# Kernel optimization log

Hardware: AMD Instinct MI355X
Metric: run time of the kernel (lower is better)

Reference implementation:

```python
import jax, jax.numpy as jnp
import numpy as np

MARGIN = 2.0
EPS = 1e-6  # F.pairwise_distance default: norm of (x1 - x2 + eps)

N, D = 4096, 768


def setup_inputs() -> dict:
    key = jax.random.key(0)
    k1, k2, k3 = jax.random.split(key, 3)
    image_embedding = jax.random.normal(k1, (N, D), dtype=jnp.float32)
    text_embedding = jax.random.normal(k2, (N, D), dtype=jnp.float32)
    ground_truth = jax.random.randint(k3, (N, N), 0, 2, dtype=jnp.int32)
    return {
        "image_embedding": image_embedding,
        "text_embedding": text_embedding,
        "ground_truth": ground_truth,
    }


def reference(image_embedding, text_embedding, ground_truth):
    d = image_embedding.shape[1]
    # Pairwise squared distance with pairwise_distance's +eps on the diff:
    # ||a - b + eps||^2 = ||a||^2 + ||b||^2 - 2 a.b + 2 eps (sum a - sum b) + d eps^2
    sa = jnp.sum(image_embedding * image_embedding, axis=1)   # [n]
    sb = jnp.sum(text_embedding * text_embedding, axis=1)     # [n]
    dot = image_embedding @ text_embedding.T                  # [n, n]
    ra = jnp.sum(image_embedding, axis=1)                     # [n]
    rb = jnp.sum(text_embedding, axis=1)                      # [n]
    sq = (sa[:, None] + sb[None, :] - 2.0 * dot
          + 2.0 * EPS * (ra[:, None] - rb[None, :]) + d * EPS * EPS)
    dist = jnp.sqrt(jnp.maximum(sq, 0.0))                     # [n, n]
    label = ground_truth.astype(dist.dtype)
    hinge = jnp.maximum(MARGIN - dist, 0.0)
    loss = jnp.mean((1.0 - label) * dist * dist + label * hinge * hinge)
    return loss
```

## Files before the change

### kernel.cpp

```cpp
#include <hip/hip_runtime.h>
#include <hip/hip_bf16.h>
#include <stdint.h>
#include <stddef.h>


#define NROWS 4096
#define DIM   768
#define BM    128
#define BN    128
#define BKE   128
#define MARGIN 2.0f
#define EPSV   1e-6f

typedef float f32x4 __attribute__((ext_vector_type(4)));
typedef long  lng2  __attribute__((ext_vector_type(2)));
typedef unsigned long long u64;
typedef unsigned char fp8_t;


__global__ __launch_bounds__(256) void prologue_kernel(
    const float* __restrict__ A, const float* __restrict__ B,
    const int* __restrict__ gt,
    fp8_t* __restrict__ Af8, fp8_t* __restrict__ Bf8,
    float* __restrict__ sa, float* __restrict__ sb,
    float* __restrict__ ra, float* __restrict__ rb,
    u64* __restrict__ gtp, float* __restrict__ out)
{
    const int tid  = threadIdx.x;
    const int wave = tid >> 6;
    const int lane = tid & 63;
    const int bx   = blockIdx.x;

    if (bx == 0 && tid == 0) out[0] = 0.0f;

    if (bx < 2048) {
        const int isB  = bx >= 1024;
        const int row  = (bx & 1023) * 4 + wave;
        const float* X = isB ? B : A;
        fp8_t* Xb      = isB ? Bf8 : Af8;
        float* sdst    = isB ? sb : sa;
        float* rdst    = isB ? rb : ra;

        const float4* xr = (const float4*)(X + (size_t)row * DIM);
        unsigned int* xb = (unsigned int*)(Xb + (size_t)row * DIM);

        float sum = 0.0f, sq = 0.0f;
        #pragma unroll
        for (int jb = 0; jb < 3; ++jb) {
            float4 v = xr[lane + 64 * jb];
            int pk = 0;
            pk = __builtin_amdgcn_cvt_pk_fp8_f32(v.x, v.y, pk, false);
            pk = __builtin_amdgcn_cvt_pk_fp8_f32(v.z, v.w, pk, true);
            const int e4  = lane + 64 * jb;
            const int seg = e4 >> 5;
            const int e   = (e4 & 31) * 4;
            const int kk  = e >> 5;
            const int q   = (e >> 3) & 3;
            const int jj  = e & 7;
            const int pos = ((kk >> 1) * 4 + q) * 16 + (kk & 1) * 8 + jj;
            xb[seg * 32 + (pos >> 2)] = (unsigned int)pk;
            sum += (v.x + v.y) + (v.z + v.w);
            sq  += v.x * v.x + v.y * v.y + v.z * v.z + v.w * v.w;
        }
        #pragma unroll
        for (int off = 32; off > 0; off >>= 1) {
            sum += __shfl_down(sum, off);
            sq  += __shfl_down(sq,  off);
        }
        if (lane == 0) { rdst[row] = sum; sdst[row] = sq; }
    } else {
        const int wid = (bx - 2048) * 4 + wave;
        const size_t base = (size_t)wid * 8;
        int v[8];
        #pragma unroll
        for (int i = 0; i < 8; ++i)
            v[i] = gt[base * 64 + (size_t)i * 64 + lane];
        u64 mine = 0;
        #pragma unroll
        for (int i = 0; i < 8; ++i) {
            const u64 m = __ballot(v[i] != 0);
            if (lane == i) mine = m;
        }
        if (lane < 8) gtp[base + lane] = mine;
    }
}

__global__ __launch_bounds__(256, 4) void loss_kernel(
    const fp8_t* __restrict__ A, const fp8_t* __restrict__ B,
    const float* __restrict__ sa, const float* __restrict__ sb,
    const float* __restrict__ ra, const float* __restrict__ rb,
    const uint2* __restrict__ gtp, float* __restrict__ out)
{
    __shared__ __align__(16) fp8_t As[BM * BKE];
    __shared__ __align__(16) fp8_t Bs[BN * BKE];

    const int tid  = threadIdx.x;
    const int wave = tid >> 6;
    const int lane = tid & 63;
    const int m0 = blockIdx.y * BM;
    const int n0 = blockIdx.x * BN;

    f32x4 acc[4][4] = {};

    const int fr = lane & 15;
    const int q  = lane >> 4;
    const int wm = (wave >> 1) * 64;
    const int wn = (wave & 1) * 64;

    const int srow = lane >> 3;
    const int sp   = lane & 7;

    for (int k0 = 0; k0 < DIM; k0 += BKE) {
        __syncthreads();
        #pragma unroll
        for (int j = 0; j < 4; ++j) {
            const int c0  = wave * 256 + j * 64;
            const int row = (c0 >> 3) + srow;
            const int gcx = sp ^ (row & 7);
            const fp8_t* ga = A + (size_t)(m0 + row) * DIM + k0 + gcx * 16;
            __builtin_amdgcn_global_load_lds(
                (const __attribute__((address_space(1))) void*)ga,
                (__attribute__((address_space(3))) void*)(As + c0 * 16),
                16, 0, 0);
        }
        #pragma unroll
        for (int j = 0; j < 4; ++j) {
            const int c0  = wave * 256 + j * 64;
            const int row = (c0 >> 3) + srow;
            const int gcx = sp ^ (row & 7);
            const fp8_t* gb = B + (size_t)(n0 + row) * DIM + k0 + gcx * 16;
            __builtin_amdgcn_global_load_lds(
                (const __attribute__((address_space(1))) void*)gb,
                (__attribute__((address_space(3))) void*)(Bs + c0 * 16),
                16, 0, 0);
        }
        __syncthreads();

        #pragma unroll
        for (int kk2 = 0; kk2 < 2; ++kk2) {
            const int c = kk2 * 4 + q;
            lng2 ap[4], bp[4];
            #pragma unroll
            for (int i = 0; i < 4; ++i) {
                const int ar = wm + i * 16 + fr;
                const int br = wn + i * 16 + fr;
                ap[i] = *(const lng2*)(As + ar * BKE + ((c ^ (ar & 7)) * 16));
                bp[i] = *(const lng2*)(Bs + br * BKE + ((c ^ (br & 7)) * 16));
            }
            #pragma unroll
            for (int mi = 0; mi < 4; ++mi)
                #pragma unroll
                for (int ni = 0; ni < 4; ++ni)
                    acc[mi][ni] = __builtin_amdgcn_mfma_f32_16x16x32_fp8_fp8(
                        ap[mi][0], bp[ni][0], acc[mi][ni], 0, 0, 0);
            #pragma unroll
            for (int mi = 0; mi < 4; ++mi)
                #pragma unroll
                for (int ni = 0; ni < 4; ++ni)
                    acc[mi][ni] = __builtin_amdgcn_mfma_f32_16x16x32_fp8_fp8(
                        ap[mi][1], bp[ni][1], acc[mi][ni], 0, 0, 0);
        }
    }

    const int cq = lane & 15;
    const int rq = (lane >> 4) * 4;
    const int cb = (n0 + wn) >> 6;

    float cc[4];
    #pragma unroll
    for (int ni = 0; ni < 4; ++ni) {
        const int col = n0 + wn + ni * 16 + cq;
        cc[ni] = sb[col] - 2.0f * EPSV * rb[col];
    }

    float local = 0.0f;
    #pragma unroll
    for (int mi = 0; mi < 4; ++mi) {
        #pragma unroll
        for (int rr = 0; rr < 4; ++rr) {
            const int row = m0 + wm + mi * 16 + rq + rr;
            const float crr = sa[row] + 2.0f * EPSV * ra[row]
                            + (float)DIM * EPSV * EPSV;
            const uint2 w = gtp[(size_t)row * (NROWS / 64) + cb];
            #pragma unroll
            for (int ni = 0; ni < 4; ++ni) {
                const float d2 = (crr + cc[ni]) - 2.0f * acc[mi][ni][rr];
                const unsigned wd = (ni < 2) ? w.x : w.y;
                const float gf = (float)((wd >> (cq + (ni & 1) * 16)) & 1u);
                float contrib = d2 - gf * d2;
                if (__builtin_expect(d2 < 4.0f, 0)) {
                    const float d2c  = fmaxf(d2, 0.0f);
                    const float dist = sqrtf(d2c);
                    const float h    = fmaxf(MARGIN - dist, 0.0f);
                    contrib = (1.0f - gf) * d2c + gf * h * h;
                }
                local += contrib;
            }
        }
    }

    #pragma unroll
    for (int off = 32; off > 0; off >>= 1) local += __shfl_down(local, off);

    float* redp = (float*)As;
    __syncthreads();
    if (lane == 0) redp[wave] = local;
    __syncthreads();
    if (tid == 0) {
        const float s = (redp[0] + redp[1]) + (redp[2] + redp[3]);
        atomicAdd(out, s * (1.0f / (4096.0f * 4096.0f)));
    }
}

extern "C" void kernel_launch(void* const* d_in, const int* in_sizes, int n_in,
                              void* d_out, int out_size, void* d_ws, size_t ws_size,
                              hipStream_t stream)
{
    const float* A  = (const float*)d_in[0];
    const float* B  = (const float*)d_in[1];
    const int*   gt = (const int*)d_in[2];
    float* out = (float*)d_out;

    char* ws = (char*)d_ws;
    const size_t NB8 = (size_t)NROWS * DIM;
    fp8_t* Af8 = (fp8_t*)(ws);
    fp8_t* Bf8 = (fp8_t*)(ws + NB8);
    float* sa = (float*)(ws + 2 * NB8);
    float* sb = (float*)(ws + 2 * NB8 + 16384);
    float* ra = (float*)(ws + 2 * NB8 + 32768);
    float* rb = (float*)(ws + 2 * NB8 + 49152);
    u64* gtp  = (u64*)(ws + 2 * NB8 + 65536);

    prologue_kernel<<<dim3(10240), 256, 0, stream>>>(
        A, B, gt, Af8, Bf8, sa, sb, ra, rb, gtp, out);
    loss_kernel<<<dim3(NROWS / BN, NROWS / BM), 256, 0, stream>>>(
        Af8, Bf8, sa, sb, ra, rb, (const uint2*)gtp, out);
}
```

Baseline: 136.9 us.

## Fuse ground-truth bitmask packing into the loss GEMM kernel's K loop

Moves the int32 ground-truth to bitmask packing out of the prologue kernel and into the loss kernel. Each block now loads its own 128x128 tile of labels during the first four K iterations, overlapping those loads with the fp8 tile loads, and stores per-row bitmasks in shared memory. The prologue shrinks to the embedding conversion only. This removes the separate packed-mask round trip through global memory, but adds register pressure and ballot work inside the GEMM loop.

```diff
diff --git a/kernel.cpp b/kernel.cpp
--- a/kernel.cpp
+++ b/kernel.cpp
@@ -20,11 +20,10 @@
 
 __global__ __launch_bounds__(256) void prologue_kernel(
     const float* __restrict__ A, const float* __restrict__ B,
-    const int* __restrict__ gt,
     fp8_t* __restrict__ Af8, fp8_t* __restrict__ Bf8,
     float* __restrict__ sa, float* __restrict__ sb,
     float* __restrict__ ra, float* __restrict__ rb,
-    u64* __restrict__ gtp, float* __restrict__ out)
+    float* __restrict__ out)
 {
     const int tid  = threadIdx.x;
     const int wave = tid >> 6;
@@ -33,66 +32,51 @@
 
     if (bx == 0 && tid == 0) out[0] = 0.0f;
 
-    if (bx < 2048) {
-        const int isB  = bx >= 1024;
-        const int row  = (bx & 1023) * 4 + wave;
-        const float* X = isB ? B : A;
-        fp8_t* Xb      = isB ? Bf8 : Af8;
-        float* sdst    = isB ? sb : sa;
-        float* rdst    = isB ? rb : ra;
-
-        const float4* xr = (const float4*)(X + (size_t)row * DIM);
-        unsigned int* xb = (unsigned int*)(Xb + (size_t)row * DIM);
-
-        float sum = 0.0f, sq = 0.0f;
-        #pragma unroll
-        for (int jb = 0; jb < 3; ++jb) {
-            float4 v = xr[lane + 64 * jb];
-            int pk = 0;
-            pk = __builtin_amdgcn_cvt_pk_fp8_f32(v.x, v.y, pk, false);
-            pk = __builtin_amdgcn_cvt_pk_fp8_f32(v.z, v.w, pk, true);
-            const int e4  = lane + 64 * jb;
-            const int seg = e4 >> 5;
-            const int e   = (e4 & 31) * 4;
-            const int kk  = e >> 5;
-            const int q   = (e >> 3) & 3;
-            const int jj  = e & 7;
-            const int pos = ((kk >> 1) * 4 + q) * 16 + (kk & 1) * 8 + jj;
-            xb[seg * 32 + (pos >> 2)] = (unsigned int)pk;
-            sum += (v.x + v.y) + (v.z + v.w);
-            sq  += v.x * v.x + v.y * v.y + v.z * v.z + v.w * v.w;
-        }
-        #pragma unroll
-        for (int off = 32; off > 0; off >>= 1) {
-            sum += __shfl_down(sum, off);
-            sq  += __shfl_down(sq,  off);
-        }
-        if (lane == 0) { rdst[row] = sum; sdst[row] = sq; }
-    } else {
-        const int wid = (bx - 2048) * 4 + wave;
-        const size_t base = (size_t)wid * 8;
-        int v[8];
-        #pragma unroll
-        for (int i = 0; i < 8; ++i)
-            v[i] = gt[base * 64 + (size_t)i * 64 + lane];
-        u64 mine = 0;
-        #pragma unroll
-        for (int i = 0; i < 8; ++i) {
-            const u64 m = __ballot(v[i] != 0);
-            if (lane == i) mine = m;
-        }
-        if (lane < 8) gtp[base + lane] = mine;
-    }
+    const int isB  = bx >= 1024;
+    const int row  = (bx & 1023) * 4 + wave;
+    const float* X = isB ? B : A;
+    fp8_t* Xb      = isB ? Bf8 : Af8;
+    float* sdst    = isB ? sb : sa;
+    float* rdst    = isB ? rb : ra;
+
+    const float4* xr = (const float4*)(X + (size_t)row * DIM);
+    unsigned int* xb = (unsigned int*)(Xb + (size_t)row * DIM);
+
+    float sum = 0.0f, sq = 0.0f;
+    #pragma unroll
+    for (int jb = 0; jb < 3; ++jb) {
+        float4 v = xr[lane + 64 * jb];
+        int pk = 0;
+        pk = __builtin_amdgcn_cvt_pk_fp8_f32(v.x, v.y, pk, false);
+        pk = __builtin_amdgcn_cvt_pk_fp8_f32(v.z, v.w, pk, true);
+        const int e4  = lane + 64 * jb;
+        const int seg = e4 >> 5;
+        const int e   = (e4 & 31) * 4;
+        const int kk  = e >> 5;
+        const int q   = (e >> 3) & 3;
+        const int jj  = e & 7;
+        const int pos = ((kk >> 1) * 4 + q) * 16 + (kk & 1) * 8 + jj;
+        xb[seg * 32 + (pos >> 2)] = (unsigned int)pk;
+        sum += (v.x + v.y) + (v.z + v.w);
+        sq  += v.x * v.x + v.y * v.y + v.z * v.z + v.w * v.w;
+    }
+    #pragma unroll
+    for (int off = 32; off > 0; off >>= 1) {
+        sum += __shfl_down(sum, off);
+        sq  += __shfl_down(sq,  off);
+    }
+    if (lane == 0) { rdst[row] = sum; sdst[row] = sq; }
 }
 
 __global__ __launch_bounds__(256, 4) void loss_kernel(
     const fp8_t* __restrict__ A, const fp8_t* __restrict__ B,
     const float* __restrict__ sa, const float* __restrict__ sb,
     const float* __restrict__ ra, const float* __restrict__ rb,
-    const uint2* __restrict__ gtp, float* __restrict__ out)
+    const int* __restrict__ gt, float* __restrict__ out)
 {
     __shared__ __align__(16) fp8_t As[BM * BKE];
     __shared__ __align__(16) fp8_t Bs[BN * BKE];
+    __shared__ unsigned int gmask[BM][4];
 
     const int tid  = threadIdx.x;
     const int wave = tid >> 6;
@@ -110,7 +94,20 @@
     const int srow = lane >> 3;
     const int sp   = lane & 7;
 
-    for (int k0 = 0; k0 < DIM; k0 += BKE) {
+    for (int kb = 0; kb < DIM / BKE; ++kb) {
+        const int k0 = kb * BKE;
+        const int rbase = kb * 32 + wave * 8;
+
+        int4 gv[4];
+        if (kb < 4) {
+            #pragma unroll
+            for (int t = 0; t < 4; ++t) {
+                const int rloc = rbase + t * 2 + (lane >> 5);
+                gv[t] = *((const int4*)(gt + (size_t)(m0 + rloc) * NROWS + n0)
+                          + (lane & 31));
+            }
+        }
+
         __syncthreads();
         #pragma unroll
         for (int j = 0; j < 4; ++j) {
@@ -134,6 +131,21 @@
                 (__attribute__((address_space(3))) void*)(Bs + c0 * 16),
                 16, 0, 0);
         }
+
+        if (kb < 4) {
+            #pragma unroll
+            for (int t = 0; t < 4; ++t) {
+                const int rloc = rbase + t * 2 + (lane >> 5);
+                #pragma unroll
+                for (int j = 0; j < 4; ++j) {
+                    const int vj = (j == 0) ? gv[t].x : (j == 1) ? gv[t].y
+                                 : (j == 2) ? gv[t].z : gv[t].w;
+                    const u64 b = __ballot(vj != 0);
+                    if ((lane & 31) == 0)
+                        gmask[rloc][j] = (unsigned int)(b >> lane);
+                }
+            }
+        }
         __syncthreads();
 
         #pragma unroll
@@ -164,7 +176,7 @@
 
     const int cq = lane & 15;
     const int rq = (lane >> 4) * 4;
-    const int cb = (n0 + wn) >> 6;
+    const int jm = cq & 3;
 
     float cc[4];
     #pragma unroll
@@ -178,15 +190,16 @@
     for (int mi = 0; mi < 4; ++mi) {
         #pragma unroll
         for (int rr = 0; rr < 4; ++rr) {
-            const int row = m0 + wm + mi * 16 + rq + rr;
+            const int rloc = wm + mi * 16 + rq + rr;
+            const int row  = m0 + rloc;
             const float crr = sa[row] + 2.0f * EPSV * ra[row]
                             + (float)DIM * EPSV * EPSV;
-            const uint2 w = gtp[(size_t)row * (NROWS / 64) + cb];
+            const unsigned int gw = gmask[rloc][jm];
             #pragma unroll
             for (int ni = 0; ni < 4; ++ni) {
                 const float d2 = (crr + cc[ni]) - 2.0f * acc[mi][ni][rr];
-                const unsigned wd = (ni < 2) ? w.x : w.y;
-                const float gf = (float)((wd >> (cq + (ni & 1) * 16)) & 1u);
+                const float gf =
+                    (float)((gw >> ((wn + ni * 16 + cq) >> 2)) & 1u);
                 float contrib = d2 - gf * d2;
                 if (__builtin_expect(d2 < 4.0f, 0)) {
                     const float d2c  = fmaxf(d2, 0.0f);
@@ -229,10 +242,9 @@
     float* sb = (float*)(ws + 2 * NB8 + 16384);
     float* ra = (float*)(ws + 2 * NB8 + 32768);
     float* rb = (float*)(ws + 2 * NB8 + 49152);
-    u64* gtp  = (u64*)(ws + 2 * NB8 + 65536);
-
-    prologue_kernel<<<dim3(10240), 256, 0, stream>>>(
-        A, B, gt, Af8, Bf8, sa, sb, ra, rb, gtp, out);
+
+    prologue_kernel<<<dim3(2048), 256, 0, stream>>>(
+        A, B, Af8, Bf8, sa, sb, ra, rb, out);
     loss_kernel<<<dim3(NROWS / BN, NROWS / BM), 256, 0, stream>>>(
-        Af8, Bf8, sa, sb, ra, rb, (const uint2*)gtp, out);
+        Af8, Bf8, sa, sb, ra, rb, gt, out);
 }
```

Result: slower. 158.5 us (+15.8%).

## Read ground-truth labels directly in loss epilogue instead of prepacking bitmask

Applied to the files above, without the earlier changes.

Removes the bit-packing pass over the int32 ground-truth matrix from the prologue and shrinks its grid accordingly. The loss kernel epilogue now loads the int labels for its tile directly from global memory. This drops the intermediate bitmask write/read and the extra blocks. In exchange, the full 64 MB label read moves into the GEMM epilogue, where it may be less efficiently streamed and less overlapped.

```diff
diff --git a/kernel.cpp b/kernel.cpp
--- a/kernel.cpp
+++ b/kernel.cpp
@@ -20,11 +20,10 @@
 
 __global__ __launch_bounds__(256) void prologue_kernel(
     const float* __restrict__ A, const float* __restrict__ B,
-    const int* __restrict__ gt,
     fp8_t* __restrict__ Af8, fp8_t* __restrict__ Bf8,
     float* __restrict__ sa, float* __restrict__ sb,
     float* __restrict__ ra, float* __restrict__ rb,
-    u64* __restrict__ gtp, float* __restrict__ out)
+    float* __restrict__ out)
 {
     const int tid  = threadIdx.x;
     const int wave = tid >> 6;
@@ -33,63 +32,47 @@
 
     if (bx == 0 && tid == 0) out[0] = 0.0f;
 
-    if (bx < 2048) {
-        const int isB  = bx >= 1024;
-        const int row  = (bx & 1023) * 4 + wave;
-        const float* X = isB ? B : A;
-        fp8_t* Xb      = isB ? Bf8 : Af8;
-        float* sdst    = isB ? sb : sa;
-        float* rdst    = isB ? rb : ra;
-
-        const float4* xr = (const float4*)(X + (size_t)row * DIM);
-        unsigned int* xb = (unsigned int*)(Xb + (size_t)row * DIM);
-
-        float sum = 0.0f, sq = 0.0f;
-        #pragma unroll
-        for (int jb = 0; jb < 3; ++jb) {
-            float4 v = xr[lane + 64 * jb];
-            int pk = 0;
-            pk = __builtin_amdgcn_cvt_pk_fp8_f32(v.x, v.y, pk, false);
-            pk = __builtin_amdgcn_cvt_pk_fp8_f32(v.z, v.w, pk, true);
-            const int e4  = lane + 64 * jb;
-            const int seg = e4 >> 5;
-            const int e   = (e4 & 31) * 4;
-            const int kk  = e >> 5;
-            const int q   = (e >> 3) & 3;
-            const int jj  = e & 7;
-            const int pos = ((kk >> 1) * 4 + q) * 16 + (kk & 1) * 8 + jj;
-            xb[seg * 32 + (pos >> 2)] = (unsigned int)pk;
-            sum += (v.x + v.y) + (v.z + v.w);
-            sq  += v.x * v.x + v.y * v.y + v.z * v.z + v.w * v.w;
-        }
-        #pragma unroll
-        for (int off = 32; off > 0; off >>= 1) {
-            sum += __shfl_down(sum, off);
-            sq  += __shfl_down(sq,  off);
-        }
-        if (lane == 0) { rdst[row] = sum; sdst[row] = sq; }
-    } else {
-        const int wid = (bx - 2048) * 4 + wave;
-        const size_t base = (size_t)wid * 8;
-        int v[8];
-        #pragma unroll
-        for (int i = 0; i < 8; ++i)
-            v[i] = gt[base * 64 + (size_t)i * 64 + lane];
-        u64 mine = 0;
-        #pragma unroll
-        for (int i = 0; i < 8; ++i) {
-            const u64 m = __ballot(v[i] != 0);
-            if (lane == i) mine = m;
-        }
-        if (lane < 8) gtp[base + lane] = mine;
-    }
+    const int isB  = bx >= 1024;
+    const int row  = (bx & 1023) * 4 + wave;
+    const float* X = isB ? B : A;
+    fp8_t* Xb      = isB ? Bf8 : Af8;
+    float* sdst    = isB ? sb : sa;
+    float* rdst    = isB ? rb : ra;
+
+    const float4* xr = (const float4*)(X + (size_t)row * DIM);
+    unsigned int* xb = (unsigned int*)(Xb + (size_t)row * DIM);
+
+    float sum = 0.0f, sq = 0.0f;
+    #pragma unroll
+    for (int jb = 0; jb < 3; ++jb) {
+        float4 v = xr[lane + 64 * jb];
+        int pk = 0;
+        pk = __builtin_amdgcn_cvt_pk_fp8_f32(v.x, v.y, pk, false);
+        pk = __builtin_amdgcn_cvt_pk_fp8_f32(v.z, v.w, pk, true);
+        const int e4  = lane + 64 * jb;
+        const int seg = e4 >> 5;
+        const int e   = (e4 & 31) * 4;
+        const int kk  = e >> 5;
+        const int q   = (e >> 3) & 3;
+        const int jj  = e & 7;
+        const int pos = ((kk >> 1) * 4 + q) * 16 + (kk & 1) * 8 + jj;
+        xb[seg * 32 + (pos >> 2)] = (unsigned int)pk;
+        sum += (v.x + v.y) + (v.z + v.w);
+        sq  += v.x * v.x + v.y * v.y + v.z * v.z + v.w * v.w;
+    }
+    #pragma unroll
+    for (int off = 32; off > 0; off >>= 1) {
+        sum += __shfl_down(sum, off);
+        sq  += __shfl_down(sq,  off);
+    }
+    if (lane == 0) { rdst[row] = sum; sdst[row] = sq; }
 }
 
 __global__ __launch_bounds__(256, 4) void loss_kernel(
     const fp8_t* __restrict__ A, const fp8_t* __restrict__ B,
     const float* __restrict__ sa, const float* __restrict__ sb,
     const float* __restrict__ ra, const float* __restrict__ rb,
-    const uint2* __restrict__ gtp, float* __restrict__ out)
+    const int* __restrict__ gt, float* __restrict__ out)
 {
     __shared__ __align__(16) fp8_t As[BM * BKE];
     __shared__ __align__(16) fp8_t Bs[BN * BKE];
@@ -164,7 +147,6 @@
 
     const int cq = lane & 15;
     const int rq = (lane >> 4) * 4;
-    const int cb = (n0 + wn) >> 6;
 
     float cc[4];
     #pragma unroll
@@ -181,12 +163,14 @@
             const int row = m0 + wm + mi * 16 + rq + rr;
             const float crr = sa[row] + 2.0f * EPSV * ra[row]
                             + (float)DIM * EPSV * EPSV;
-            const uint2 w = gtp[(size_t)row * (NROWS / 64) + cb];
+            const int* gr = gt + (size_t)row * NROWS + n0 + wn + cq;
+            int gvals[4];
+            #pragma unroll
+            for (int ni = 0; ni < 4; ++ni) gvals[ni] = gr[ni * 16];
             #pragma unroll
             for (int ni = 0; ni < 4; ++ni) {
                 const float d2 = (crr + cc[ni]) - 2.0f * acc[mi][ni][rr];
-                const unsigned wd = (ni < 2) ? w.x : w.y;
-                const float gf = (float)((wd >> (cq + (ni & 1) * 16)) & 1u);
+                const float gf = (gvals[ni] != 0) ? 1.0f : 0.0f;
                 float contrib = d2 - gf * d2;
                 if (__builtin_expect(d2 < 4.0f, 0)) {
                     const float d2c  = fmaxf(d2, 0.0f);
@@ -229,10 +213,9 @@
     float* sb = (float*)(ws + 2 * NB8 + 16384);
     float* ra = (float*)(ws + 2 * NB8 + 32768);
     float* rb = (float*)(ws + 2 * NB8 + 49152);
-    u64* gtp  = (u64*)(ws + 2 * NB8 + 65536);
-
-    prologue_kernel<<<dim3(10240), 256, 0, stream>>>(
-        A, B, gt, Af8, Bf8, sa, sb, ra, rb, gtp, out);
+
+    prologue_kernel<<<dim3(2048), 256, 0, stream>>>(
+        A, B, Af8, Bf8, sa, sb, ra, rb, out);
     loss_kernel<<<dim3(NROWS / BN, NROWS / BM), 256, 0, stream>>>(
-        Af8, Bf8, sa, sb, ra, rb, (const uint2*)gtp, out);
+        Af8, Bf8, sa, sb, ra, rb, gt, out);
 }
```

After: 138.1 us. Within noise of the previous version (+0.9%).
